# Optimization experiments

Hardware: AMD Instinct MI355X
Metric: run time of the kernel (lower is better)

Reference implementation:

```python
import jax, jax.numpy as jnp
import numpy as np

B, C, P, HP, WP = 128, 3, 196, 16, 16  # batch, channels, patches, patch h, patch w
E = 768  # embedding size; patches_pixel_count = C*HP*WP = 768


def setup_inputs() -> dict:
    key = jax.random.key(0)
    ks = jax.random.split(key, 9)
    return {
        "inputs": jax.random.normal(ks[0], (B, C, P, HP, WP), dtype=jnp.float32),
        "W1": jax.random.normal(ks[1], (C * HP * WP, 32), dtype=jnp.float32) * 0.02,
        "b1": jax.random.normal(ks[2], (32,), dtype=jnp.float32) * 0.02,
        "W2": jax.random.normal(ks[3], (32, 64), dtype=jnp.float32) * 0.02,
        "b2": jax.random.normal(ks[4], (64,), dtype=jnp.float32) * 0.02,
        "W3": jax.random.normal(ks[5], (64, E), dtype=jnp.float32) * 0.02,
        "b3": jax.random.normal(ks[6], (E,), dtype=jnp.float32) * 0.02,
        "cls_token": jax.random.normal(ks[7], (1, E), dtype=jnp.float32) * 0.02,
        "pos_enc": jax.random.normal(ks[8], (P + 1, E), dtype=jnp.float32) * 0.02,
    }


def reference(inputs, W1, b1, W2, b2, W3, b3, cls_token, pos_enc):
    b, c, p, hp, wp = inputs.shape
    # per-patch slab is [C, hp, wp] flattened in (C, h, w) order -> [B, P, C*hp*wp]
    x = jnp.transpose(inputs, (0, 2, 1, 3, 4)).reshape(b, p, c * hp * wp)
    x = x @ W1 + b1          # [B, P, 32]
    x = x @ W2 + b2          # [B, P, 64]
    x = x @ W3 + b3          # [B, P, E]
    cls = jnp.broadcast_to(cls_token[None], (b, 1, cls_token.shape[-1]))
    x = jnp.concatenate([cls, x], axis=1)  # [B, P+1, E]
    return x + pos_enc[None]               # broadcast add of position encodings
```

## Files before the change

kernel.cpp:

```cpp
#include <hip/hip_runtime.h>


#define BATCH 128
#define CH    3
#define NP    196
#define PIX   256
#define K1    768
#define N1    32
#define N2    64
#define EMB   768
#define TM    32

typedef __bf16 bf16x8 __attribute__((ext_vector_type(8)));
typedef float  f32x4  __attribute__((ext_vector_type(4)));

#define W1T_OFF  0
#define W2T_OFF  49152
#define W3T_OFF  (49152 + 4096)
#define POSB_OFF (53248 + 98304)

__global__ void patchembed_prep(const float* __restrict__ W1, const float* __restrict__ W2,
                                const float* __restrict__ W3, const float* __restrict__ b3,
                                const float* __restrict__ cls, const float* __restrict__ pos,
                                __bf16* __restrict__ w1t, __bf16* __restrict__ w2t,
                                __bf16* __restrict__ w3t, float* __restrict__ posb,
                                float* __restrict__ out)
{
    int i = blockIdx.x * blockDim.x + threadIdx.x;
    const int T1 = K1 * N1;
    const int T2 = T1 + N1 * N2;
    const int T3 = T2 + N2 * EMB;
    const int T4 = T3 + 197 * EMB;
    const int T5 = T4 + BATCH * EMB;

    if (i < T1) {
        int n = i / K1, k = i - n * K1;
        w1t[i] = (__bf16)W1[k * N1 + n];
    } else if (i < T2) {
        int j = i - T1;
        int n = j / N1, k = j - n * N1;
        w2t[j] = (__bf16)W2[k * N2 + n];
    } else if (i < T3) {
        int j = i - T2;
        int n = j / N2, k = j - n * N2;
        w3t[j] = (__bf16)W3[k * EMB + n];
    } else if (i < T4) {
        int j = i - T3;
        int r = j / EMB, c = j - r * EMB;
        float base = (r == 0) ? cls[c] : b3[c];
        posb[j] = base + pos[j];
    } else if (i < T5) {
        int j = i - T4;
        int b = j / EMB, c = j - b * EMB;
        out[b * (197 * EMB) + c] = cls[c] + pos[c];
    }
}

__global__ __launch_bounds__(256) void patchembed_main(
    const float* __restrict__ X,
    const float* __restrict__ b1,
    const float* __restrict__ b2,
    const __bf16* __restrict__ w1t,
    const __bf16* __restrict__ w2t,
    const __bf16* __restrict__ w3t,
    const float* __restrict__ posb,
    float* __restrict__ out)
{
    __shared__ __align__(16) __bf16 h1s[TM][40];
    __shared__ __align__(16) __bf16 h2s[TM][72];

    const int tid  = threadIdx.x;
    const int wv   = tid >> 6;
    const int lane = tid & 63;
    const int l15  = lane & 15;
    const int quad = lane >> 4;
    const int r0   = blockIdx.x * TM;

    {
        const int mi = wv >> 1;
        const int ni = wv & 1;
        const int m   = mi * 16 + l15;
        const int row = r0 + m;
        const int b   = row / NP;
        const int p   = row - b * NP;
        const int base0 = ((b * CH) * NP + p) * PIX;
        const __bf16* wrow = w1t + (ni * 16 + l15) * K1;

        f32x4 acc = {0.f, 0.f, 0.f, 0.f};
        #pragma unroll 4
        for (int kb = 0; kb < 24; ++kb) {
            const int c      = kb >> 3;
            const int within = (kb & 7) * 32 + quad * 8;
            const float4* xp = (const float4*)(X + base0 + c * (NP * PIX) + within);
            float4 u = xp[0];
            float4 v = xp[1];
            bf16x8 a;
            a[0] = (__bf16)u.x; a[1] = (__bf16)u.y; a[2] = (__bf16)u.z; a[3] = (__bf16)u.w;
            a[4] = (__bf16)v.x; a[5] = (__bf16)v.y; a[6] = (__bf16)v.z; a[7] = (__bf16)v.w;
            bf16x8 bf = *(const bf16x8*)(wrow + kb * 32 + quad * 8);
            acc = __builtin_amdgcn_mfma_f32_16x16x32_bf16(a, bf, acc, 0, 0, 0);
        }
        const float bias = b1[ni * 16 + l15];
        #pragma unroll
        for (int r = 0; r < 4; ++r)
            h1s[mi * 16 + quad * 4 + r][ni * 16 + l15] = (__bf16)(acc[r] + bias);
    }
    __syncthreads();

    {
        bf16x8 bf = *(const bf16x8*)(w2t + (wv * 16 + l15) * N1 + quad * 8);
        bf16x8 a0 = *(const bf16x8*)(&h1s[l15][quad * 8]);
        bf16x8 a1 = *(const bf16x8*)(&h1s[16 + l15][quad * 8]);
        f32x4 z = {0.f, 0.f, 0.f, 0.f};
        f32x4 acc0 = __builtin_amdgcn_mfma_f32_16x16x32_bf16(a0, bf, z, 0, 0, 0);
        f32x4 acc1 = __builtin_amdgcn_mfma_f32_16x16x32_bf16(a1, bf, z, 0, 0, 0);
        const float bias = b2[wv * 16 + l15];
        #pragma unroll
        for (int r = 0; r < 4; ++r) {
            h2s[quad * 4 + r][wv * 16 + l15]      = (__bf16)(acc0[r] + bias);
            h2s[16 + quad * 4 + r][wv * 16 + l15] = (__bf16)(acc1[r] + bias);
        }
    }
    __syncthreads();

    {
        bf16x8 a00 = *(const bf16x8*)(&h2s[l15][quad * 8]);
        bf16x8 a01 = *(const bf16x8*)(&h2s[l15][32 + quad * 8]);
        bf16x8 a10 = *(const bf16x8*)(&h2s[16 + l15][quad * 8]);
        bf16x8 a11 = *(const bf16x8*)(&h2s[16 + l15][32 + quad * 8]);

        int obase[2][4];
        int pbase[2][4];
        #pragma unroll
        for (int mi2 = 0; mi2 < 2; ++mi2)
            #pragma unroll
            for (int r = 0; r < 4; ++r) {
                const int row = r0 + mi2 * 16 + quad * 4 + r;
                const int b = row / NP;
                const int p = row - b * NP;
                obase[mi2][r] = (b * 197 + p + 1) * EMB;
                pbase[mi2][r] = (p + 1) * EMB;
            }

        for (int t = 0; t < 12; ++t) {
            const int nt  = wv * 12 + t;
            const int col = nt * 16 + l15;
            const __bf16* wr = w3t + col * N2;
            bf16x8 bf0 = *(const bf16x8*)(wr + quad * 8);
            bf16x8 bf1 = *(const bf16x8*)(wr + 32 + quad * 8);
            f32x4 z = {0.f, 0.f, 0.f, 0.f};
            f32x4 c0 = __builtin_amdgcn_mfma_f32_16x16x32_bf16(a00, bf0, z, 0, 0, 0);
            c0       = __builtin_amdgcn_mfma_f32_16x16x32_bf16(a01, bf1, c0, 0, 0, 0);
            f32x4 c1 = __builtin_amdgcn_mfma_f32_16x16x32_bf16(a10, bf0, z, 0, 0, 0);
            c1       = __builtin_amdgcn_mfma_f32_16x16x32_bf16(a11, bf1, c1, 0, 0, 0);
            #pragma unroll
            for (int r = 0; r < 4; ++r) {
                out[obase[0][r] + col] = c0[r] + posb[pbase[0][r] + col];
                out[obase[1][r] + col] = c1[r] + posb[pbase[1][r] + col];
            }
        }
    }
}

extern "C" void kernel_launch(void* const* d_in, const int* in_sizes, int n_in,
                              void* d_out, int out_size, void* d_ws, size_t ws_size,
                              hipStream_t stream)
{
    const float* X   = (const float*)d_in[0];
    const float* W1  = (const float*)d_in[1];
    const float* b1  = (const float*)d_in[2];
    const float* W2  = (const float*)d_in[3];
    const float* b2  = (const float*)d_in[4];
    const float* W3  = (const float*)d_in[5];
    const float* b3  = (const float*)d_in[6];
    const float* cls = (const float*)d_in[7];
    const float* pos = (const float*)d_in[8];
    float* out = (float*)d_out;

    char* ws = (char*)d_ws;
    __bf16* w1t = (__bf16*)(ws + W1T_OFF);
    __bf16* w2t = (__bf16*)(ws + W2T_OFF);
    __bf16* w3t = (__bf16*)(ws + W3T_OFF);
    float*  posb = (float*)(ws + POSB_OFF);

    patchembed_prep<<<1271, 256, 0, stream>>>(W1, W2, W3, b3, cls, pos,
                                              w1t, w2t, w3t, posb, out);
    patchembed_main<<<784, 256, 0, stream>>>(X, b1, b2, w1t, w2t, w3t, posb, out);
}
```

Measured before the change: 184.1 us.

## Split layer-1 K dimension across waves with 16-row tiles and doubled grid

Each block now handles 16 patch rows instead of 32, and the first GEMM's K=768 reduction is split across the four waves, each covering 6 k-steps for both 32-wide output halves. Partial sums are reduced through fp32 shared memory before layer 2. The grid doubles to 1568 blocks so more blocks can run concurrently and hide the latency of the input reads. In exchange, every block reloads the full W2/W3 weights for half as many rows and performs an extra shared-memory reduction.

```diff
diff --git a/kernel.cpp b/kernel.cpp
--- a/kernel.cpp
+++ b/kernel.cpp
@@ -9,7 +9,6 @@
 #define N1    32
 #define N2    64
 #define EMB   768
-#define TM    32
 
 typedef __bf16 bf16x8 __attribute__((ext_vector_type(8)));
 typedef float  f32x4  __attribute__((ext_vector_type(4)));
@@ -66,97 +65,102 @@
     const float* __restrict__ posb,
     float* __restrict__ out)
 {
-    __shared__ __align__(16) __bf16 h1s[TM][40];
-    __shared__ __align__(16) __bf16 h2s[TM][72];
+    __shared__ __align__(16) float  h1p[4][16][36];
+    __shared__ __align__(16) __bf16 h2s[16][72];
 
     const int tid  = threadIdx.x;
     const int wv   = tid >> 6;
     const int lane = tid & 63;
     const int l15  = lane & 15;
-    const int quad = lane >> 4;
-    const int r0   = blockIdx.x * TM;
+    const int q    = lane >> 4;
+    const int r0   = blockIdx.x * 16;
 
     {
-        const int mi = wv >> 1;
-        const int ni = wv & 1;
-        const int m   = mi * 16 + l15;
-        const int row = r0 + m;
-        const int b   = row / NP;
-        const int p   = row - b * NP;
+        const int xrow  = r0 + l15;
+        const int b     = xrow / NP;
+        const int p     = xrow - b * NP;
         const int base0 = ((b * CH) * NP + p) * PIX;
-        const __bf16* wrow = w1t + (ni * 16 + l15) * K1;
+        const __bf16* w0r = w1t + l15 * K1;
+        const __bf16* w1r = w1t + (16 + l15) * K1;
 
-        f32x4 acc = {0.f, 0.f, 0.f, 0.f};
-        #pragma unroll 4
-        for (int kb = 0; kb < 24; ++kb) {
-            const int c      = kb >> 3;
-            const int within = (kb & 7) * 32 + quad * 8;
-            const float4* xp = (const float4*)(X + base0 + c * (NP * PIX) + within);
+        f32x4 acc0 = {0.f, 0.f, 0.f, 0.f};
+        f32x4 acc1 = {0.f, 0.f, 0.f, 0.f};
+        #pragma unroll
+        for (int t = 0; t < 6; ++t) {
+            const int kb  = wv * 6 + t;
+            const int c   = kb >> 3;
+            const int off = (kb & 7) * 32 + q * 8;
+            const float4* xp = (const float4*)(X + base0 + c * (NP * PIX) + off);
             float4 u = xp[0];
             float4 v = xp[1];
             bf16x8 a;
             a[0] = (__bf16)u.x; a[1] = (__bf16)u.y; a[2] = (__bf16)u.z; a[3] = (__bf16)u.w;
             a[4] = (__bf16)v.x; a[5] = (__bf16)v.y; a[6] = (__bf16)v.z; a[7] = (__bf16)v.w;
-            bf16x8 bf = *(const bf16x8*)(wrow + kb * 32 + quad * 8);
-            acc = __builtin_amdgcn_mfma_f32_16x16x32_bf16(a, bf, acc, 0, 0, 0);
+            bf16x8 f0 = *(const bf16x8*)(w0r + kb * 32 + q * 8);
+            bf16x8 f1 = *(const bf16x8*)(w1r + kb * 32 + q * 8);
+            acc0 = __builtin_amdgcn_mfma_f32_16x16x32_bf16(a, f0, acc0, 0, 0, 0);
+            acc1 = __builtin_amdgcn_mfma_f32_16x16x32_bf16(a, f1, acc1, 0, 0, 0);
         }
-        const float bias = b1[ni * 16 + l15];
-        #pragma unroll
-        for (int r = 0; r < 4; ++r)
-            h1s[mi * 16 + quad * 4 + r][ni * 16 + l15] = (__bf16)(acc[r] + bias);
-    }
-    __syncthreads();
-
-    {
-        bf16x8 bf = *(const bf16x8*)(w2t + (wv * 16 + l15) * N1 + quad * 8);
-        bf16x8 a0 = *(const bf16x8*)(&h1s[l15][quad * 8]);
-        bf16x8 a1 = *(const bf16x8*)(&h1s[16 + l15][quad * 8]);
-        f32x4 z = {0.f, 0.f, 0.f, 0.f};
-        f32x4 acc0 = __builtin_amdgcn_mfma_f32_16x16x32_bf16(a0, bf, z, 0, 0, 0);
-        f32x4 acc1 = __builtin_amdgcn_mfma_f32_16x16x32_bf16(a1, bf, z, 0, 0, 0);
-        const float bias = b2[wv * 16 + l15];
         #pragma unroll
         for (int r = 0; r < 4; ++r) {
-            h2s[quad * 4 + r][wv * 16 + l15]      = (__bf16)(acc0[r] + bias);
-            h2s[16 + quad * 4 + r][wv * 16 + l15] = (__bf16)(acc1[r] + bias);
+            h1p[wv][q * 4 + r][l15]      = acc0[r];
+            h1p[wv][q * 4 + r][16 + l15] = acc1[r];
         }
     }
     __syncthreads();
 
     {
-        bf16x8 a00 = *(const bf16x8*)(&h2s[l15][quad * 8]);
-        bf16x8 a01 = *(const bf16x8*)(&h2s[l15][32 + quad * 8]);
-        bf16x8 a10 = *(const bf16x8*)(&h2s[16 + l15][quad * 8]);
-        bf16x8 a11 = *(const bf16x8*)(&h2s[16 + l15][32 + quad * 8]);
+        f32x4 s0 = {0.f, 0.f, 0.f, 0.f};
+        f32x4 s1 = {0.f, 0.f, 0.f, 0.f};
+        #pragma unroll
+        for (int w = 0; w < 4; ++w) {
+            s0 += *(const f32x4*)&h1p[w][l15][q * 8];
+            s1 += *(const f32x4*)&h1p[w][l15][q * 8 + 4];
+        }
+        s0 += *(const f32x4*)(b1 + q * 8);
+        s1 += *(const f32x4*)(b1 + q * 8 + 4);
+        bf16x8 a;
+        #pragma unroll
+        for (int j = 0; j < 4; ++j) {
+            a[j]     = (__bf16)s0[j];
+            a[4 + j] = (__bf16)s1[j];
+        }
+        bf16x8 f = *(const bf16x8*)(w2t + (wv * 16 + l15) * N1 + q * 8);
+        f32x4 z = {0.f, 0.f, 0.f, 0.f};
+        f32x4 h2 = __builtin_amdgcn_mfma_f32_16x16x32_bf16(a, f, z, 0, 0, 0);
+        const float bias = b2[wv * 16 + l15];
+        #pragma unroll
+        for (int r = 0; r < 4; ++r)
+            h2s[q * 4 + r][wv * 16 + l15] = (__bf16)(h2[r] + bias);
+    }
+    __syncthreads();
 
-        int obase[2][4];
-        int pbase[2][4];
+    {
+        bf16x8 a0 = *(const bf16x8*)(&h2s[l15][q * 8]);
+        bf16x8 a1 = *(const bf16x8*)(&h2s[l15][32 + q * 8]);
+
+        int obase[4], pbase[4];
         #pragma unroll
-        for (int mi2 = 0; mi2 < 2; ++mi2)
+        for (int r = 0; r < 4; ++r) {
+            const int row = r0 + q * 4 + r;
+            const int b = row / NP;
+            const int p = row - b * NP;
+            obase[r] = (b * 197 + p + 1) * EMB;
+            pbase[r] = (p + 1) * EMB;
+        }
+
+        #pragma unroll 4
+        for (int t = 0; t < 12; ++t) {
+            const int col = wv * 192 + t * 16 + l15;
+            const __bf16* wr = w3t + col * N2;
+            bf16x8 f0 = *(const bf16x8*)(wr + q * 8);
+            bf16x8 f1 = *(const bf16x8*)(wr + 32 + q * 8);
+            f32x4 z = {0.f, 0.f, 0.f, 0.f};
+            f32x4 c0 = __builtin_amdgcn_mfma_f32_16x16x32_bf16(a0, f0, z, 0, 0, 0);
+            c0       = __builtin_amdgcn_mfma_f32_16x16x32_bf16(a1, f1, c0, 0, 0, 0);
             #pragma unroll
             for (int r = 0; r < 4; ++r) {
-                const int row = r0 + mi2 * 16 + quad * 4 + r;
-                const int b = row / NP;
-                const int p = row - b * NP;
-                obase[mi2][r] = (b * 197 + p + 1) * EMB;
-                pbase[mi2][r] = (p + 1) * EMB;
-            }
-
-        for (int t = 0; t < 12; ++t) {
-            const int nt  = wv * 12 + t;
-            const int col = nt * 16 + l15;
-            const __bf16* wr = w3t + col * N2;
-            bf16x8 bf0 = *(const bf16x8*)(wr + quad * 8);
-            bf16x8 bf1 = *(const bf16x8*)(wr + 32 + quad * 8);
-            f32x4 z = {0.f, 0.f, 0.f, 0.f};
-            f32x4 c0 = __builtin_amdgcn_mfma_f32_16x16x32_bf16(a00, bf0, z, 0, 0, 0);
-            c0       = __builtin_amdgcn_mfma_f32_16x16x32_bf16(a01, bf1, c0, 0, 0, 0);
-            f32x4 c1 = __builtin_amdgcn_mfma_f32_16x16x32_bf16(a10, bf0, z, 0, 0, 0);
-            c1       = __builtin_amdgcn_mfma_f32_16x16x32_bf16(a11, bf1, c1, 0, 0, 0);
-            #pragma unroll
-            for (int r = 0; r < 4; ++r) {
-                out[obase[0][r] + col] = c0[r] + posb[pbase[0][r] + col];
-                out[obase[1][r] + col] = c1[r] + posb[pbase[1][r] + col];
+                out[obase[0 * 4 + r] + col] = c0[r] + posb[pbase[r] + col];
             }
         }
     }
@@ -185,5 +189,5 @@
 
     patchembed_prep<<<1271, 256, 0, stream>>>(W1, W2, W3, b3, cls, pos,
                                               w1t, w2t, w3t, posb, out);
-    patchembed_main<<<784, 256, 0, stream>>>(X, b1, b2, w1t, w2t, w3t, posb, out);
+    patchembed_main<<<1568, 256, 0, stream>>>(X, b1, b2, w1t, w2t, w3t, posb, out);
 }
```

New measurement: 183.7 us. No clear change (-0.3%).
